# Performance work log

Measured on AMD Instinct MI355X. Metric: run time of the kernel, lower is better.

Reference implementation:

```python
import jax, jax.numpy as jnp
import numpy as np

NU, NI, DIN, DOUT, NS, E = 100000, 100000, 128, 128, 5, 500000


def setup_inputs() -> dict:
    key = jax.random.key(0)
    ks = jax.random.split(key, 9)
    scale = 1.0 / np.sqrt(DIN)
    return {
        "user_inputs": jax.random.normal(ks[0], (NU, DIN), jnp.float32),
        "item_inputs": jax.random.normal(ks[1], (NI, DIN), jnp.float32),
        "weight": jax.random.normal(ks[2], (DIN, DOUT, NS), jnp.float32) * scale,
        "u_rows": jax.random.randint(ks[3], (NS, E), 0, NU),
        "u_cols": jax.random.randint(ks[4], (NS, E), 0, NI),
        "u_vals": jax.random.uniform(ks[5], (NS, E), jnp.float32),
        "i_rows": jax.random.randint(ks[6], (NS, E), 0, NI),
        "i_cols": jax.random.randint(ks[7], (NS, E), 0, NU),
        "i_vals": jax.random.uniform(ks[8], (NS, E), jnp.float32),
    }


def _spmm(rows, cols, vals, dense, n_rows):
    # COO sparse [n_rows, n_cols] @ dense [n_cols, d] -> [n_rows, d]
    msgs = vals[:, None] * dense[cols]  # [E, d]
    return jax.ops.segment_sum(msgs, rows, num_segments=n_rows)


def reference(user_inputs, item_inputs, weight, u_rows, u_cols, u_vals, i_rows, i_cols, i_vals):
    n_users = user_inputs.shape[0]
    n_items = item_inputs.shape[0]
    num_support = weight.shape[-1]
    w = jnp.zeros(weight.shape[:2], weight.dtype)
    user_hidden = jnp.zeros((n_users, weight.shape[1]), weight.dtype)
    item_hidden = jnp.zeros((n_items, weight.shape[1]), weight.dtype)
    for i in range(num_support):  # fixed small structural loop (5 rating levels)
        w = w + weight[..., i]            # cumulative weight sum, as in original
        tmp_u = user_inputs @ w           # [NU, DOUT]
        tmp_v = item_inputs @ w           # [NI, DOUT]
        user_hidden = user_hidden + _spmm(u_rows[i], u_cols[i], u_vals[i], tmp_v, n_users)
        item_hidden = item_hidden + _spmm(i_rows[i], i_cols[i], i_vals[i], tmp_u, n_items)
    return jax.nn.relu(user_hidden), jax.nn.relu(item_hidden)
```

## Files before the change

kernel.cpp:

```cpp
#include <hip/hip_runtime.h>

#define R_     100000
#define NSUP   5
#define EDGES  500000
#define D_     128
#define ND     (NSUP * D_)
#define BR     64
#define PPS2   ((R_ + BR - 1) / BR)
#define NBIN1  PPS2
#define CAP2   512

#define EPB    8192
#define BPS    62
#define OROWS  1568

using short8 = __attribute__((ext_vector_type(8))) short;
using f32x4  = __attribute__((ext_vector_type(4))) float;

static __device__ __forceinline__ float bf2f_lo(unsigned p) { return __uint_as_float(p << 16); }
static __device__ __forceinline__ float bf2f_hi(unsigned p) { return __uint_as_float(p & 0xffff0000u); }
static __device__ __forceinline__ unsigned short f2bf(float x) {
    unsigned u = __float_as_uint(x);
    return (unsigned short)((u + 0x7fffu + ((u >> 16) & 1u)) >> 16);
}

__global__ __launch_bounds__(256) void prep_k(const float* __restrict__ user_in,
                                              const float* __restrict__ item_in,
                                              const float* __restrict__ w,
                                              unsigned short* __restrict__ srcb,
                                              unsigned short* __restrict__ bt) {
    int b = blockIdx.x, tid = threadIdx.x;
    if (b < 25000) {
        int side = b / 12500;
        int t = (b - side * 12500) * 256 + tid;
        const float* src = side ? user_in : item_in;
        float4 v = *(const float4*)(src + (size_t)t * 4);
        ushort4 o;
        o.x = f2bf(v.x); o.y = f2bf(v.y); o.z = f2bf(v.z); o.w = f2bf(v.w);
        *(ushort4*)(srcb + (size_t)side * (R_ * D_) + (size_t)t * 4) = o;
    } else {
        int t = (b - 25000) * 256 + tid;
        int o = t / ND;
        int kk = t - o * ND;
        int i = kk >> 7, d = kk & 127;
        float s = 0.f;
        for (int j = 0; j <= i; j++) s += w[(d * D_ + o) * NSUP + j];
        bt[t] = f2bf(s);
    }
}

__global__ __launch_bounds__(512) void place2_k(const int* __restrict__ u_rows,
                                                const int* __restrict__ u_cols,
                                                const float* __restrict__ u_vals,
                                                const int* __restrict__ i_rows,
                                                const int* __restrict__ i_cols,
                                                const float* __restrict__ i_vals,
                                                int* __restrict__ offs2,
                                                uint2* __restrict__ cedge2) {
    __shared__ int   hist[NBIN1];
    __shared__ int   part[512];
    __shared__ uint2 estage[EPB];

    int seg = blockIdx.x / BPS;
    int bb  = blockIdx.x - seg * BPS;
    int side = seg / NSUP;
    int sup  = seg - side * NSUP;
    const int*   rows = side ? i_rows : u_rows;
    const int*   cols = side ? i_cols : u_cols;
    const float* vals = side ? i_vals : u_vals;
    int e0 = bb * EPB;
    int ecnt = EDGES - e0; if (ecnt > EPB) ecnt = EPB;
    size_t gb = (size_t)sup * EDGES + e0;
    int tid = threadIdx.x;

    for (int b = tid; b < NBIN1; b += 512) hist[b] = 0;
    __syncthreads();
    for (int e = tid; e < ecnt; e += 512)
        atomicAdd(&hist[rows[gb + e] >> 6], 1);
    __syncthreads();
    int b0 = tid * 4, s4 = 0;
    if (b0 < NBIN1) {
#pragma unroll
        for (int k = 0; k < 4; k++)
            if (b0 + k < NBIN1) s4 += hist[b0 + k];
    }
    part[tid] = s4;
    __syncthreads();
    for (int off = 1; off < 512; off <<= 1) {
        int u = (tid >= off) ? part[tid - off] : 0;
        __syncthreads();
        part[tid] += u;
        __syncthreads();
    }
    int ex = part[tid] - s4;
    int orow = seg * OROWS;
    if (b0 < NBIN1) {
        int run = ex;
#pragma unroll
        for (int k = 0; k < 4; k++) {
            int b = b0 + k;
            if (b < NBIN1) {
                int c = hist[b];
                offs2[(size_t)(orow + b) * 64 + bb] = run;
                hist[b] = run;
                run += c;
            }
        }
    }
    if (tid == 0) offs2[(size_t)(orow + NBIN1) * 64 + bb] = ecnt;
    __syncthreads();
    for (int e = tid; e < ecnt; e += 512) {
        int r = rows[gb + e];
        int pos = atomicAdd(&hist[r >> 6], 1);
        uint2 E;
        E.x = (unsigned)cols[gb + e] | ((unsigned)(r & 63) << 17);
        E.y = __float_as_uint(vals[gb + e]);
        estage[pos] = E;
    }
    __syncthreads();
    size_t cbase = (size_t)(seg * BPS + bb) * EPB;
    for (int e = tid; e < ecnt; e += 512) cedge2[cbase + e] = estage[e];
}

__global__ __launch_bounds__(256) void rowsort_k(const int* __restrict__ offs2,
                                                 const uint2* __restrict__ cedge2,
                                                 uint2* __restrict__ cedge3,
                                                 int* __restrict__ rtab) {
    __shared__ uint2 eraw[CAP2];
    __shared__ uint2 eds[CAP2];
    __shared__ int rstart[BPS + 1];
    __shared__ int ro0[BPS];
    __shared__ int rcnt[BR];
    __shared__ int rsc[BR];

    int q = blockIdx.x;
    int seg = q / PPS2;
    int bin = q - seg * PPS2;
    int side = seg / NSUP;
    int sup  = seg - side * NSUP;
    int tid = threadIdx.x;
    int wid = tid >> 6, lane = tid & 63;

    if (wid == 0) {
        int o0v = 0, cnt = 0;
        if (lane < BPS) {
            const int* orow = offs2 + ((size_t)seg * OROWS + bin) * 64;
            o0v = orow[lane];
            cnt = orow[64 + lane] - o0v;
        }
        int s = cnt;
#pragma unroll
        for (int off = 1; off < 64; off <<= 1) {
            int u = __shfl_up(s, off, 64);
            if (lane >= off) s += u;
        }
        if (lane < BPS) { rstart[lane] = s - cnt; ro0[lane] = o0v; }
        if (lane == BPS - 1) rstart[BPS] = s;
    } else if (wid == 1 && lane < BR) {
        rcnt[lane] = 0;
    }
    __syncthreads();
    int n = rstart[BPS]; if (n > CAP2) n = CAP2;
    if (tid < 4 * BPS) {
        int rb = tid >> 2, j0 = tid & 3;
        int rs = rstart[rb];
        int cnt = rstart[rb + 1] - rs;
        const uint2* src = cedge2 + (size_t)(seg * BPS + rb) * EPB + ro0[rb];
        for (int j = j0; j < cnt; j += 4) {
            int pos = rs + j;
            if (pos < CAP2) eraw[pos] = src[j];
        }
    }
    __syncthreads();
    for (int e = tid; e < n; e += 256)
        atomicAdd(&rcnt[(eraw[e].x >> 17) & 63], 1);
    __syncthreads();
    if (wid == 0) {
        int vv = rcnt[lane];
        int s = vv;
#pragma unroll
        for (int off = 1; off < 64; off <<= 1) {
            int u = __shfl_up(s, off, 64);
            if (lane >= off) s += u;
        }
        rsc[lane] = s;
        rcnt[lane] = s - vv;
    }
    __syncthreads();
    if (tid < BR) {
        int v = rsc[tid]; if (v > CAP2) v = CAP2;
        rtab[((size_t)(side * PPS2 + bin)) * (NSUP * BR) + sup * BR + tid] = v;
    }
    for (int e = tid; e < n; e += 256) {
        uint2 E = eraw[e];
        int pos = atomicAdd(&rcnt[(E.x >> 17) & 63], 1);
        if (pos < CAP2) eds[pos] = E;
    }
    __syncthreads();
    size_t cb = (size_t)q * CAP2;
    for (int e = tid; e < n; e += 256) cedge3[cb + e] = eds[e];
}

__global__ __launch_bounds__(512, 8) void fused_k(const uint2* __restrict__ cedge3,
                                                  const int* __restrict__ rtab,
                                                  const unsigned short* __restrict__ srcb,
                                                  const unsigned short* __restrict__ BT,
                                                  float* __restrict__ out) {
    __shared__ unsigned short stile[BR * D_];
    __shared__ uint2 eds[CAP2];
    __shared__ int rsc_all[NSUP * BR];

    int side = blockIdx.x / PPS2;
    int bin  = blockIdx.x - side * PPS2;
    const unsigned short* srcbf = srcb + (size_t)side * (R_ * D_);
    float* outp = out + (size_t)side * R_ * D_;

    int tid = threadIdx.x;
    int wid = tid >> 6, lane = tid & 63;
    int g = lane >> 4, l16 = lane & 15;

    if (tid < NSUP * BR)
        rsc_all[tid] = rtab[((size_t)(side * PPS2 + bin)) * (NSUP * BR) + tid];

    f32x4 acc[4];
#pragma unroll
    for (int rt = 0; rt < 4; rt++) acc[rt] = (f32x4){0.f, 0.f, 0.f, 0.f};

    for (int i = 0; i < NSUP; i++) {
        int seg = side * NSUP + i;
        __syncthreads();
        int n = rsc_all[i * BR + 63];
        const uint2* ebase = cedge3 + (size_t)(seg * PPS2 + bin) * CAP2;
        for (int e = tid; e < n; e += 512) eds[e] = ebase[e];
        __syncthreads();

        for (int rq = wid; rq < 16; rq += 8) {
            int r = rq * 4 + g;
            int s0 = r ? rsc_all[i * BR + r - 1] : 0;
            int e2 = rsc_all[i * BR + r];
            float a0 = 0.f, a1 = 0.f, a2 = 0.f, a3 = 0.f;
            float a4 = 0.f, a5 = 0.f, a6 = 0.f, a7 = 0.f;
            int e = s0;
            for (; e + 1 < e2; e += 2) {
                uint2 E0 = eds[e], E1 = eds[e + 1];
                const uint4 p0 = *(const uint4*)(srcbf + (size_t)(E0.x & 0x1FFFFu) * D_ + l16 * 8);
                const uint4 p1 = *(const uint4*)(srcbf + (size_t)(E1.x & 0x1FFFFu) * D_ + l16 * 8);
                float v0 = __uint_as_float(E0.y), v1 = __uint_as_float(E1.y);
                a0 += v0 * bf2f_lo(p0.x); a1 += v0 * bf2f_hi(p0.x);
                a2 += v0 * bf2f_lo(p0.y); a3 += v0 * bf2f_hi(p0.y);
                a4 += v0 * bf2f_lo(p0.z); a5 += v0 * bf2f_hi(p0.z);
                a6 += v0 * bf2f_lo(p0.w); a7 += v0 * bf2f_hi(p0.w);
                a0 += v1 * bf2f_lo(p1.x); a1 += v1 * bf2f_hi(p1.x);
                a2 += v1 * bf2f_lo(p1.y); a3 += v1 * bf2f_hi(p1.y);
                a4 += v1 * bf2f_lo(p1.z); a5 += v1 * bf2f_hi(p1.z);
                a6 += v1 * bf2f_lo(p1.w); a7 += v1 * bf2f_hi(p1.w);
            }
            for (; e < e2; e++) {
                uint2 E = eds[e];
                const uint4 pk = *(const uint4*)(srcbf + (size_t)(E.x & 0x1FFFFu) * D_ + l16 * 8);
                float vv = __uint_as_float(E.y);
                a0 += vv * bf2f_lo(pk.x); a1 += vv * bf2f_hi(pk.x);
                a2 += vv * bf2f_lo(pk.y); a3 += vv * bf2f_hi(pk.y);
                a4 += vv * bf2f_lo(pk.z); a5 += vv * bf2f_hi(pk.z);
                a6 += vv * bf2f_lo(pk.w); a7 += vv * bf2f_hi(pk.w);
            }
            uint4 P;
            P.x = ((unsigned)f2bf(a1) << 16) | f2bf(a0);
            P.y = ((unsigned)f2bf(a3) << 16) | f2bf(a2);
            P.z = ((unsigned)f2bf(a5) << 16) | f2bf(a4);
            P.w = ((unsigned)f2bf(a7) << 16) | f2bf(a6);
            int boff = r * 256 + ((l16 * 16) ^ ((r & 7) << 4));
            *(uint4*)((char*)stile + boff) = P;
        }
        __syncthreads();

        const unsigned short* btp = BT + (size_t)(wid * 16 + l16) * ND + i * D_;
#pragma unroll
        for (int cc = 0; cc < 4; cc++) {
            short8 b = *(const short8*)(btp + cc * 32 + g * 8);
#pragma unroll
            for (int rt = 0; rt < 4; rt++) {
                int row = rt * 16 + l16;
                int boff = row * 256 + ((cc * 64 + g * 16) ^ ((row & 7) << 4));
                short8 afr = *(const short8*)((const char*)stile + boff);
                acc[rt] = __builtin_amdgcn_mfma_f32_16x16x32_bf16(afr, b, acc[rt], 0, 0, 0);
            }
        }
    }

#pragma unroll
    for (int rt = 0; rt < 4; rt++) {
#pragma unroll
        for (int rr = 0; rr < 4; rr++) {
            int grow = bin * BR + rt * 16 + g * 4 + rr;
            if (grow < R_) {
                int col = wid * 16 + l16;
                float v = acc[rt][rr];
                outp[(size_t)grow * D_ + col] = v > 0.f ? v : 0.f;
            }
        }
    }
}

extern "C" void kernel_launch(void* const* d_in, const int* in_sizes, int n_in,
                              void* d_out, int out_size, void* d_ws, size_t ws_size,
                              hipStream_t stream) {
    const float* user_in = (const float*)d_in[0];
    const float* item_in = (const float*)d_in[1];
    const float* weight  = (const float*)d_in[2];
    const int* u_rows = (const int*)d_in[3];
    const int* u_cols = (const int*)d_in[4];
    const float* u_vals = (const float*)d_in[5];
    const int* i_rows = (const int*)d_in[6];
    const int* i_cols = (const int*)d_in[7];
    const float* i_vals = (const float*)d_in[8];
    float* out = (float*)d_out;

    char* ws = (char*)d_ws;
    unsigned short* srcb = (unsigned short*)(ws);
    unsigned short* BT   = (unsigned short*)(ws + 51200000);
    uint2* cedge2        = (uint2*)         (ws + 51363840);
    int*   offs2         = (int*)           (ws + 91996160);
    uint2* cedge3        = (uint2*)         (ws + 96010240);
    int*   rtab          = (int*)           (ws + 160030720);

    prep_k<<<25320, 256, 0, stream>>>(user_in, item_in, weight, srcb, BT);
    place2_k<<<10 * BPS, 512, 0, stream>>>(u_rows, u_cols, u_vals,
                                           i_rows, i_cols, i_vals, offs2, cedge2);
    rowsort_k<<<10 * PPS2, 256, 0, stream>>>(offs2, cedge2, cedge3, rtab);
    fused_k<<<2 * PPS2, 512, 0, stream>>>(cedge3, rtab, srcb, BT, out);
}
```

Baseline: 557.1 us.

## Merge prep and placement kernels, halve edge chunks, preload all supports, coalesce output

Merges the bf16 conversion, weight-prefix, and edge bucketing kernels into one launch so they overlap. Edge chunks are halved so more blocks run placement in parallel, and the block-wide LDS scan becomes a wavefront shuffle scan. The fused kernel now preloads all five supports' edges into shared memory up front and unrolls the gather loop by four for more memory-level parallelism. Output goes through an LDS transpose for coalesced float4 stores. The merged kernel uses more shared memory per block for the conversion blocks, and the larger LDS footprint in the fused kernel may lower occupancy.

```diff
diff --git a/kernel.cpp b/kernel.cpp
--- a/kernel.cpp
+++ b/kernel.cpp
@@ -10,9 +10,13 @@
 #define NBIN1  PPS2
 #define CAP2   512
 
-#define EPB    8192
-#define BPS    62
-#define OROWS  1568
+#define EPB    4096
+#define BPS    123
+#define OST    128
+#define OROWS  (NBIN1 + 1)
+
+#define PPB    12500
+#define BTB    160
 
 using short8 = __attribute__((ext_vector_type(8))) short;
 using f32x4  = __attribute__((ext_vector_type(4))) float;
@@ -24,45 +28,47 @@
     return (unsigned short)((u + 0x7fffu + ((u >> 16) & 1u)) >> 16);
 }
 
-__global__ __launch_bounds__(256) void prep_k(const float* __restrict__ user_in,
-                                              const float* __restrict__ item_in,
-                                              const float* __restrict__ w,
-                                              unsigned short* __restrict__ srcb,
-                                              unsigned short* __restrict__ bt) {
+__global__ __launch_bounds__(512) void pp_k(const float* __restrict__ user_in,
+                                            const float* __restrict__ item_in,
+                                            const float* __restrict__ w,
+                                            const int* __restrict__ u_rows,
+                                            const int* __restrict__ u_cols,
+                                            const float* __restrict__ u_vals,
+                                            const int* __restrict__ i_rows,
+                                            const int* __restrict__ i_cols,
+                                            const float* __restrict__ i_vals,
+                                            unsigned short* __restrict__ srcb,
+                                            unsigned short* __restrict__ bt,
+                                            int* __restrict__ offs2,
+                                            uint2* __restrict__ cedge2) {
+    __shared__ uint2 estage[EPB];
+    __shared__ int   hist[NBIN1];
+    __shared__ int   wsum[8];
+
     int b = blockIdx.x, tid = threadIdx.x;
-    if (b < 25000) {
-        int side = b / 12500;
-        int t = (b - side * 12500) * 256 + tid;
+    if (b < PPB) {
+        int side = b / 6250;
+        int t = (b - side * 6250) * 512 + tid;
         const float* src = side ? user_in : item_in;
         float4 v = *(const float4*)(src + (size_t)t * 4);
         ushort4 o;
         o.x = f2bf(v.x); o.y = f2bf(v.y); o.z = f2bf(v.z); o.w = f2bf(v.w);
         *(ushort4*)(srcb + (size_t)side * (R_ * D_) + (size_t)t * 4) = o;
-    } else {
-        int t = (b - 25000) * 256 + tid;
+        return;
+    }
+    if (b < PPB + BTB) {
+        int t = (b - PPB) * 512 + tid;
         int o = t / ND;
         int kk = t - o * ND;
         int i = kk >> 7, d = kk & 127;
         float s = 0.f;
         for (int j = 0; j <= i; j++) s += w[(d * D_ + o) * NSUP + j];
         bt[t] = f2bf(s);
-    }
-}
-
-__global__ __launch_bounds__(512) void place2_k(const int* __restrict__ u_rows,
-                                                const int* __restrict__ u_cols,
-                                                const float* __restrict__ u_vals,
-                                                const int* __restrict__ i_rows,
-                                                const int* __restrict__ i_cols,
-                                                const float* __restrict__ i_vals,
-                                                int* __restrict__ offs2,
-                                                uint2* __restrict__ cedge2) {
-    __shared__ int   hist[NBIN1];
-    __shared__ int   part[512];
-    __shared__ uint2 estage[EPB];
-
-    int seg = blockIdx.x / BPS;
-    int bb  = blockIdx.x - seg * BPS;
+        return;
+    }
+    int q = b - (PPB + BTB);
+    int seg = q / BPS;
+    int bb  = q - seg * BPS;
     int side = seg / NSUP;
     int sup  = seg - side * NSUP;
     const int*   rows = side ? i_rows : u_rows;
@@ -71,43 +77,43 @@
     int e0 = bb * EPB;
     int ecnt = EDGES - e0; if (ecnt > EPB) ecnt = EPB;
     size_t gb = (size_t)sup * EDGES + e0;
-    int tid = threadIdx.x;
-
-    for (int b = tid; b < NBIN1; b += 512) hist[b] = 0;
+
+    for (int j = tid; j < NBIN1; j += 512) hist[j] = 0;
     __syncthreads();
     for (int e = tid; e < ecnt; e += 512)
         atomicAdd(&hist[rows[gb + e] >> 6], 1);
     __syncthreads();
-    int b0 = tid * 4, s4 = 0;
+    int b0 = tid * 4;
+    int c0 = 0, c1 = 0, c2 = 0, c3 = 0, s4 = 0;
     if (b0 < NBIN1) {
-#pragma unroll
-        for (int k = 0; k < 4; k++)
-            if (b0 + k < NBIN1) s4 += hist[b0 + k];
-    }
-    part[tid] = s4;
-    __syncthreads();
-    for (int off = 1; off < 512; off <<= 1) {
-        int u = (tid >= off) ? part[tid - off] : 0;
-        __syncthreads();
-        part[tid] += u;
-        __syncthreads();
-    }
-    int ex = part[tid] - s4;
+        c0 = hist[b0];
+        c1 = (b0 + 1 < NBIN1) ? hist[b0 + 1] : 0;
+        c2 = (b0 + 2 < NBIN1) ? hist[b0 + 2] : 0;
+        c3 = (b0 + 3 < NBIN1) ? hist[b0 + 3] : 0;
+        s4 = c0 + c1 + c2 + c3;
+    }
+    int lane = tid & 63, wv = tid >> 6;
+    int s = s4;
+#pragma unroll
+    for (int off = 1; off < 64; off <<= 1) {
+        int u = __shfl_up(s, off, 64);
+        if (lane >= off) s += u;
+    }
+    if (lane == 63) wsum[wv] = s;
+    __syncthreads();
+    int woff = 0;
+#pragma unroll
+    for (int k = 0; k < 8; k++) woff += (k < wv) ? wsum[k] : 0;
+    int ex = woff + s - s4;
     int orow = seg * OROWS;
     if (b0 < NBIN1) {
         int run = ex;
-#pragma unroll
-        for (int k = 0; k < 4; k++) {
-            int b = b0 + k;
-            if (b < NBIN1) {
-                int c = hist[b];
-                offs2[(size_t)(orow + b) * 64 + bb] = run;
-                hist[b] = run;
-                run += c;
-            }
-        }
-    }
-    if (tid == 0) offs2[(size_t)(orow + NBIN1) * 64 + bb] = ecnt;
+        offs2[(size_t)(orow + b0) * OST + bb] = run;  hist[b0] = run;  run += c0;
+        if (b0 + 1 < NBIN1) { offs2[(size_t)(orow + b0 + 1) * OST + bb] = run; hist[b0 + 1] = run; run += c1; }
+        if (b0 + 2 < NBIN1) { offs2[(size_t)(orow + b0 + 2) * OST + bb] = run; hist[b0 + 2] = run; run += c2; }
+        if (b0 + 3 < NBIN1) { offs2[(size_t)(orow + b0 + 3) * OST + bb] = run; hist[b0 + 3] = run; run += c3; }
+    }
+    if (tid == 0) offs2[(size_t)(orow + NBIN1) * OST + bb] = ecnt;
     __syncthreads();
     for (int e = tid; e < ecnt; e += 512) {
         int r = rows[gb + e];
@@ -142,31 +148,33 @@
     int wid = tid >> 6, lane = tid & 63;
 
     if (wid == 0) {
-        int o0v = 0, cnt = 0;
-        if (lane < BPS) {
-            const int* orow = offs2 + ((size_t)seg * OROWS + bin) * 64;
-            o0v = orow[lane];
-            cnt = orow[64 + lane] - o0v;
-        }
-        int s = cnt;
+        const int* orow = offs2 + ((size_t)seg * OROWS + bin) * OST;
+        int j0 = lane * 2, j1 = lane * 2 + 1;
+        int o0 = 0, o1 = 0, cc0 = 0, cc1 = 0;
+        if (j0 < BPS) { o0 = orow[j0]; cc0 = orow[j0 + OST] - o0; }
+        if (j1 < BPS) { o1 = orow[j1]; cc1 = orow[j1 + OST] - o1; }
+        int sc = cc0 + cc1;
+        int s = sc;
 #pragma unroll
         for (int off = 1; off < 64; off <<= 1) {
             int u = __shfl_up(s, off, 64);
             if (lane >= off) s += u;
         }
-        if (lane < BPS) { rstart[lane] = s - cnt; ro0[lane] = o0v; }
-        if (lane == BPS - 1) rstart[BPS] = s;
+        int ex = s - sc;
+        if (j0 < BPS) { rstart[j0] = ex; ro0[j0] = o0; }
+        if (j1 < BPS) { rstart[j1] = ex + cc0; ro0[j1] = o1; }
+        if (lane == 63) rstart[BPS] = s;
     } else if (wid == 1 && lane < BR) {
         rcnt[lane] = 0;
     }
     __syncthreads();
     int n = rstart[BPS]; if (n > CAP2) n = CAP2;
-    if (tid < 4 * BPS) {
-        int rb = tid >> 2, j0 = tid & 3;
+    if (tid < 2 * BPS) {
+        int rb = tid >> 1, j0 = tid & 1;
         int rs = rstart[rb];
         int cnt = rstart[rb + 1] - rs;
         const uint2* src = cedge2 + (size_t)(seg * BPS + rb) * EPB + ro0[rb];
-        for (int j = j0; j < cnt; j += 4) {
+        for (int j = j0; j < cnt; j += 2) {
             int pos = rs + j;
             if (pos < CAP2) eraw[pos] = src[j];
         }
@@ -207,7 +215,7 @@
                                                   const unsigned short* __restrict__ BT,
                                                   float* __restrict__ out) {
     __shared__ unsigned short stile[BR * D_];
-    __shared__ uint2 eds[CAP2];
+    __shared__ uint2 eds5[NSUP * CAP2];
     __shared__ int rsc_all[NSUP * BR];
 
     int side = blockIdx.x / PPS2;
@@ -219,21 +227,23 @@
     int wid = tid >> 6, lane = tid & 63;
     int g = lane >> 4, l16 = lane & 15;
 
-    if (tid < NSUP * BR)
-        rsc_all[tid] = rtab[((size_t)(side * PPS2 + bin)) * (NSUP * BR) + tid];
+    size_t rbase = ((size_t)(side * PPS2 + bin)) * (NSUP * BR);
+    if (tid < NSUP * BR) rsc_all[tid] = rtab[rbase + tid];
+#pragma unroll
+    for (int i = 0; i < NSUP; i++) {
+        int n = rtab[rbase + i * BR + 63]; if (n > CAP2) n = CAP2;
+        const uint2* ebase = cedge3 + (size_t)((side * NSUP + i) * PPS2 + bin) * CAP2;
+        for (int e = tid; e < n; e += 512) eds5[i * CAP2 + e] = ebase[e];
+    }
 
     f32x4 acc[4];
 #pragma unroll
     for (int rt = 0; rt < 4; rt++) acc[rt] = (f32x4){0.f, 0.f, 0.f, 0.f};
 
+    __syncthreads();
+
     for (int i = 0; i < NSUP; i++) {
-        int seg = side * NSUP + i;
-        __syncthreads();
-        int n = rsc_all[i * BR + 63];
-        const uint2* ebase = cedge3 + (size_t)(seg * PPS2 + bin) * CAP2;
-        for (int e = tid; e < n; e += 512) eds[e] = ebase[e];
-        __syncthreads();
-
+        const uint2* eds = eds5 + i * CAP2;
         for (int rq = wid; rq < 16; rq += 8) {
             int r = rq * 4 + g;
             int s0 = r ? rsc_all[i * BR + r - 1] : 0;
@@ -241,11 +251,14 @@
             float a0 = 0.f, a1 = 0.f, a2 = 0.f, a3 = 0.f;
             float a4 = 0.f, a5 = 0.f, a6 = 0.f, a7 = 0.f;
             int e = s0;
-            for (; e + 1 < e2; e += 2) {
-                uint2 E0 = eds[e], E1 = eds[e + 1];
+            for (; e + 3 < e2; e += 4) {
+                uint2 E0 = eds[e], E1 = eds[e + 1], E2 = eds[e + 2], E3 = eds[e + 3];
                 const uint4 p0 = *(const uint4*)(srcbf + (size_t)(E0.x & 0x1FFFFu) * D_ + l16 * 8);
                 const uint4 p1 = *(const uint4*)(srcbf + (size_t)(E1.x & 0x1FFFFu) * D_ + l16 * 8);
+                const uint4 p2 = *(const uint4*)(srcbf + (size_t)(E2.x & 0x1FFFFu) * D_ + l16 * 8);
+                const uint4 p3 = *(const uint4*)(srcbf + (size_t)(E3.x & 0x1FFFFu) * D_ + l16 * 8);
                 float v0 = __uint_as_float(E0.y), v1 = __uint_as_float(E1.y);
+                float v2 = __uint_as_float(E2.y), v3 = __uint_as_float(E3.y);
                 a0 += v0 * bf2f_lo(p0.x); a1 += v0 * bf2f_hi(p0.x);
                 a2 += v0 * bf2f_lo(p0.y); a3 += v0 * bf2f_hi(p0.y);
                 a4 += v0 * bf2f_lo(p0.z); a5 += v0 * bf2f_hi(p0.z);
@@ -254,6 +267,14 @@
                 a2 += v1 * bf2f_lo(p1.y); a3 += v1 * bf2f_hi(p1.y);
                 a4 += v1 * bf2f_lo(p1.z); a5 += v1 * bf2f_hi(p1.z);
                 a6 += v1 * bf2f_lo(p1.w); a7 += v1 * bf2f_hi(p1.w);
+                a0 += v2 * bf2f_lo(p2.x); a1 += v2 * bf2f_hi(p2.x);
+                a2 += v2 * bf2f_lo(p2.y); a3 += v2 * bf2f_hi(p2.y);
+                a4 += v2 * bf2f_lo(p2.z); a5 += v2 * bf2f_hi(p2.z);
+                a6 += v2 * bf2f_lo(p2.w); a7 += v2 * bf2f_hi(p2.w);
+                a0 += v3 * bf2f_lo(p3.x); a1 += v3 * bf2f_hi(p3.x);
+                a2 += v3 * bf2f_lo(p3.y); a3 += v3 * bf2f_hi(p3.y);
+                a4 += v3 * bf2f_lo(p3.z); a5 += v3 * bf2f_hi(p3.z);
+                a6 += v3 * bf2f_lo(p3.w); a7 += v3 * bf2f_hi(p3.w);
             }
             for (; e < e2; e++) {
                 uint2 E = eds[e];
@@ -277,28 +298,45 @@
         const unsigned short* btp = BT + (size_t)(wid * 16 + l16) * ND + i * D_;
 #pragma unroll
         for (int cc = 0; cc < 4; cc++) {
-            short8 b = *(const short8*)(btp + cc * 32 + g * 8);
+            short8 bfr = *(const short8*)(btp + cc * 32 + g * 8);
 #pragma unroll
             for (int rt = 0; rt < 4; rt++) {
                 int row = rt * 16 + l16;
                 int boff = row * 256 + ((cc * 64 + g * 16) ^ ((row & 7) << 4));
                 short8 afr = *(const short8*)((const char*)stile + boff);
-                acc[rt] = __builtin_amdgcn_mfma_f32_16x16x32_bf16(afr, b, acc[rt], 0, 0, 0);
-            }
-        }
-    }
-
-#pragma unroll
-    for (int rt = 0; rt < 4; rt++) {
-#pragma unroll
-        for (int rr = 0; rr < 4; rr++) {
-            int grow = bin * BR + rt * 16 + g * 4 + rr;
+                acc[rt] = __builtin_amdgcn_mfma_f32_16x16x32_bf16(afr, bfr, acc[rt], 0, 0, 0);
+            }
+        }
+        __syncthreads();
+    }
+
+    float* ltile = (float*)stile;
+#pragma unroll
+    for (int half = 0; half < 2; half++) {
+#pragma unroll
+        for (int rt2 = 0; rt2 < 2; rt2++) {
+#pragma unroll
+            for (int rr = 0; rr < 4; rr++) {
+                int lrow = rt2 * 16 + g * 4 + rr;
+                float v = acc[half * 2 + rt2][rr];
+                v = v > 0.f ? v : 0.f;
+                *(float*)((char*)ltile + lrow * 512 +
+                          (((wid * 16 + l16) * 4) ^ ((lrow & 7) << 4))) = v;
+            }
+        }
+        __syncthreads();
+#pragma unroll
+        for (int s = 0; s < 2; s++) {
+            int idx = tid + s * 512;
+            int lrow = idx >> 5, c4 = idx & 31;
+            int grow = bin * BR + half * 32 + lrow;
             if (grow < R_) {
-                int col = wid * 16 + l16;
-                float v = acc[rt][rr];
-                outp[(size_t)grow * D_ + col] = v > 0.f ? v : 0.f;
-            }
-        }
+                float4 v = *(const float4*)((const char*)ltile + lrow * 512 +
+                                            ((c4 * 16) ^ ((lrow & 7) << 4)));
+                *(float4*)(outp + (size_t)grow * D_ + c4 * 4) = v;
+            }
+        }
+        __syncthreads();
     }
 }
 
@@ -320,13 +358,14 @@
     unsigned short* srcb = (unsigned short*)(ws);
     unsigned short* BT   = (unsigned short*)(ws + 51200000);
     uint2* cedge2        = (uint2*)         (ws + 51363840);
-    int*   offs2         = (int*)           (ws + 91996160);
-    uint2* cedge3        = (uint2*)         (ws + 96010240);
-    int*   rtab          = (int*)           (ws + 160030720);
-
-    prep_k<<<25320, 256, 0, stream>>>(user_in, item_in, weight, srcb, BT);
-    place2_k<<<10 * BPS, 512, 0, stream>>>(u_rows, u_cols, u_vals,
-                                           i_rows, i_cols, i_vals, offs2, cedge2);
+    int*   offs2         = (int*)           (ws + 91668480);
+    uint2* cedge3        = (uint2*)         (ws + 99676160);
+    int*   rtab          = (int*)           (ws + 163696640);
+
+    pp_k<<<PPB + BTB + 10 * BPS, 512, 0, stream>>>(user_in, item_in, weight,
+                                                   u_rows, u_cols, u_vals,
+                                                   i_rows, i_cols, i_vals,
+                                                   srcb, BT, offs2, cedge2);
     rowsort_k<<<10 * PPS2, 256, 0, stream>>>(offs2, cedge2, cedge3, rtab);
     fused_k<<<2 * PPS2, 512, 0, stream>>>(cedge3, rtab, srcb, BT, out);
 }
```

Measured after the change: 537.5 us. -3.5%, faster.
